# Performance work log

Hardware: AMD Instinct MI355X
Metric: run time of the kernel (lower is better)

The kernel has to match this reference:

```python
import jax, jax.numpy as jnp
import numpy as np

C, NC, B, T, H, W = 64, 4, 4, 8, 96, 96
BT = B * T
_DN = ('NCDHW', 'OIDHW', 'NCDHW')


def setup_inputs() -> dict:
    key = jax.random.key(0)
    ks = jax.random.split(key, 16)
    r = lambda i, shape, s=0.02: jax.random.normal(ks[i], shape, jnp.float32) * s
    f32 = jnp.float32
    return {
        'x': jax.random.normal(ks[0], (BT, C, H, W), f32),
        't': T,
        'temporal_kernels': r(1, (NC, C)),            # (num_components, C) per-channel kernel scale
        'kernel_weights': jnp.ones((NC,), f32),
        'length_scales': jnp.ones((NC,), f32),
        'temporal_basis': r(2, (C, T)),               # (C, 8) learned temporal basis
        'sc_w1': r(3, (C // 8, C), 0.05), 'sc_b1': jnp.zeros((C // 8,), f32),
        'sc_w2': r(4, (2 * C, C // 8), 0.05), 'sc_b2': jnp.zeros((2 * C,), f32),
        'diff_w': r(5, (C, 1, 3, 1, 1), 0.1),         # depthwise temporal conv
        'diff_gamma': jnp.ones((C,), f32), 'diff_beta': jnp.zeros((C,), f32),
        'diff_mean': r(6, (C,), 0.1),
        'diff_var': jnp.ones((C,), f32) + 0.1 * jax.random.uniform(ks[7], (C,), f32),
        'unc_w1': r(8, (C // 4, C), 0.05), 'unc_b1': jnp.zeros((C // 4,), f32),
        'unc_w2': r(9, (2, C // 4), 0.05), 'unc_b2': jnp.zeros((2,), f32),
        'pool_w': r(10, (C, C, 3, 1, 1), 0.02), 'pool_b': jnp.zeros((C,), f32),
        'proj_w': r(11, (C, C), 0.05),                # spectral-normalized 1x1x1 conv
        'bn_gamma': jnp.ones((C,), f32), 'bn_beta': jnp.zeros((C,), f32),
        'bn_mean': r(12, (C,), 0.1),
        'bn_var': jnp.ones((C,), f32) + 0.1 * jax.random.uniform(ks[13], (C,), f32),
        'temperature': jnp.float32(1.0),
    }


def _bc(v):
    return v[None, :, None, None, None]


def reference(x, t, temporal_kernels, kernel_weights, length_scales, temporal_basis,
              sc_w1, sc_b1, sc_w2, sc_b2,
              diff_w, diff_gamma, diff_beta, diff_mean, diff_var,
              unc_w1, unc_b1, unc_w2, unc_b2,
              pool_w, pool_b, proj_w,
              bn_gamma, bn_beta, bn_mean, bn_var, temperature):
    bt, c, h, w = x.shape
    b = bt // t
    x5 = x.reshape(b, t, c, h, w).transpose(0, 2, 1, 3, 4)   # (b,c,t,h,w)

    # --- Gaussian process temporal attention: per-channel (t,t) RBF mixture kernel ---
    ti = jnp.arange(t, dtype=x.dtype)
    dt2 = (ti[:, None] - ti[None, :]) ** 2                    # (t,t)
    ls = jnp.exp(length_scales)                               # (nc,)
    rbf = jnp.exp(-dt2[None] / (2.0 * ls[:, None, None] ** 2))  # (nc,t,t)
    wts = jax.nn.softmax(kernel_weights)
    K = jnp.einsum('i,ic,ist->cst', wts, temporal_kernels, rbf)  # (c,t,t)
    gp = jnp.einsum('cst,bctn->bcsn', K, x5.reshape(b, c, t, h * w)).reshape(b, c, t, h, w)

    # --- stochastic temporal sampling (eval: deterministic importance mask) ---
    mask = jax.nn.softmax(temporal_basis.mean(axis=0))        # (t,)
    stoch = x5 * mask[None, None, :, None, None]

    # --- spatial covariance gate (global pooled MLP -> sigmoid gate) ---
    g = x5.mean(axis=(2, 3, 4))                               # (b,c)
    h1 = jax.nn.gelu(g @ sc_w1.T + sc_b1, approximate=False)
    cov = h1 @ sc_w2.T + sc_b2                                # (b,2c); second half = cov_var
    cov_w = jax.nn.sigmoid(cov[:, c:])[:, :, None, None, None]
    fused0 = gp * cov_w + stoch * (1.0 - cov_w)

    # --- diffusion: depthwise temporal conv + BN(eval) + GELU ---
    d = jax.lax.conv_general_dilated(fused0, diff_w, (1, 1, 1), ((1, 1), (0, 0), (0, 0)),
                                     dimension_numbers=_DN, feature_group_count=c)
    d = _bc(diff_gamma) * (d - _bc(diff_mean)) / jnp.sqrt(_bc(diff_var) + 1e-5) + _bc(diff_beta)
    d = jax.nn.gelu(d, approximate=False)

    # --- uncertainty head + precision-weighted fusion ---
    u = jax.nn.gelu(jnp.einsum('bcthw,oc->bothw', d, unc_w1) + _bc(unc_b1), approximate=False)
    u = jnp.einsum('bcthw,oc->bothw', u, unc_w2) + _bc(unc_b2)  # (b,2,t,h,w)
    mu, var = u[:, :1], u[:, 1:]
    prec = 1.0 / (var + 1e-6)
    fused = (mu * prec + d) / (prec + 1.0)

    # --- temporal pool: temporal conv then global spatial mean ---
    p = jax.lax.conv_general_dilated(fused, pool_w, (1, 1, 1), ((1, 1), (0, 0), (0, 0)),
                                     dimension_numbers=_DN) + _bc(pool_b)
    out = fused + p.mean(axis=(3, 4), keepdims=True)

    # --- spectral-normalized 1x1x1 projection + BN(eval) ---
    sigma = jnp.linalg.svd(proj_w, compute_uv=False)[0]
    out = jnp.einsum('bcthw,oc->bothw', out, proj_w / sigma)
    out = _bc(bn_gamma) * (out - _bc(bn_mean)) / jnp.sqrt(_bc(bn_var) + 1e-5) + _bc(bn_beta)

    out = out.transpose(0, 2, 1, 3, 4).reshape(bt, c, h, w)
    return x + jnp.tanh(temperature) * out
```

## Files before the change

kernel.cpp:

```cpp
#include <hip/hip_runtime.h>
#include <math.h>

#define C64 64
#define NCK 4
#define BB  4
#define TT  8
#define HH  96
#define WW  96
#define HW  9216
#define CHW (C64*HW)
#define NTILE 32
#define NBLK_PER_B (HW/NTILE)

#define OFF_GSUM 0
#define OFF_S    256
#define OFF_COVW 2304
#define OFF_K    2560
#define OFF_MASK 6656
#define OFF_AC   6664
#define OFF_BC   6728
#define OFF_P2   6792
#define OFF_B2   10888
#define OFF_BIAS3 10952
#define OFF_P2BF 13000
#define OFF_P2T  15048
#define OFF_POOLT 19144
#define ZERO_N   2304

typedef __attribute__((ext_vector_type(8))) short short8;
typedef __attribute__((ext_vector_type(4))) float f32x4;

__device__ __forceinline__ float gelu_f(float v) {
    return 0.5f * v * (1.0f + erff(v * 0.70710678118654752f));
}
__device__ __forceinline__ unsigned short f2bf(float f) {
    union { float f; unsigned int u; } v; v.f = f;
    unsigned int r = (v.u + 0x7fffu + ((v.u >> 16) & 1u)) >> 16;
    return (unsigned short)r;
}
__device__ __forceinline__ float bf2f(unsigned short h) {
    union { unsigned int u; float f; } v; v.u = ((unsigned int)h) << 16;
    return v.f;
}
__device__ __forceinline__ int swz(int tn, int c) {
    return (tn << 6) + (c ^ ((tn & 7) << 3));
}

__global__ __launch_bounds__(256) void k1_gsum(const float* __restrict__ x,
                                               float* __restrict__ ws) {
    const int blk = blockIdx.x;
    const float4* p = reinterpret_cast<const float4*>(x + (size_t)blk * HW);
    float s = 0.f;
    for (int i = threadIdx.x; i < HW / 4; i += 256) {
        float4 v = p[i];
        s += v.x + v.y + v.z + v.w;
    }
    #pragma unroll
    for (int off = 32; off; off >>= 1) s += __shfl_down(s, off, 64);
    __shared__ float part[4];
    const int wid = threadIdx.x >> 6, lane = threadIdx.x & 63;
    if (lane == 0) part[wid] = s;
    __syncthreads();
    if (threadIdx.x == 0) {
        float t = part[0] + part[1] + part[2] + part[3];
        int c = blk % C64;
        int b = (blk / C64) / TT;
        atomicAdd(ws + OFF_GSUM + b * C64 + c, t);
    }
}

__global__ __launch_bounds__(256) void k2_prep(
    const float* __restrict__ tk, const float* __restrict__ kw,
    const float* __restrict__ lsc, const float* __restrict__ tb,
    const float* __restrict__ sc_w1, const float* __restrict__ sc_b1,
    const float* __restrict__ sc_w2, const float* __restrict__ sc_b2,
    const float* __restrict__ diff_gamma, const float* __restrict__ diff_beta,
    const float* __restrict__ diff_mean, const float* __restrict__ diff_var,
    const float* __restrict__ proj_w, const float* __restrict__ pool_w,
    const float* __restrict__ bn_gamma, const float* __restrict__ bn_beta,
    const float* __restrict__ bn_mean, const float* __restrict__ bn_var,
    const float* __restrict__ temperature,
    float* __restrict__ ws) {
    __shared__ float gsh[BB * C64];
    __shared__ float h1[BB][8];
    __shared__ float wtss[NCK], lss[NCK];
    __shared__ float Pls[64 * 64];
    __shared__ float Msh[64 * 64];
    __shared__ float M2sh[64 * 64];
    __shared__ float v0[64], v1[64];
    __shared__ float lamsh;
    const int tid = threadIdx.x;

    gsh[tid] = ws[OFF_GSUM + tid] * (1.0f / ((float)TT * (float)HW));
    for (int q = tid; q < 4096; q += 256) Pls[q] = proj_w[q];
    __syncthreads();

    if (tid < BB * 8) {
        int b = tid >> 3, j = tid & 7;
        float a = sc_b1[j];
        for (int c = 0; c < C64; c++) a += gsh[b * C64 + c] * sc_w1[j * C64 + c];
        h1[b][j] = gelu_f(a);
    }
    if (tid == 0) {
        float mx = -1e30f;
        for (int i = 0; i < NCK; i++) mx = fmaxf(mx, kw[i]);
        float e[NCK], s = 0.f;
        for (int i = 0; i < NCK; i++) { e[i] = expf(kw[i] - mx); s += e[i]; }
        for (int i = 0; i < NCK; i++) { wtss[i] = e[i] / s; lss[i] = expf(lsc[i]); }
    }
    if (tid == 1) {
        float m[TT], mx = -1e30f;
        for (int t = 0; t < TT; t++) {
            float a = 0.f;
            for (int c = 0; c < C64; c++) a += tb[c * TT + t];
            m[t] = a * (1.0f / (float)C64);
            mx = fmaxf(mx, m[t]);
        }
        float s = 0.f;
        for (int t = 0; t < TT; t++) { m[t] = expf(m[t] - mx); s += m[t]; }
        for (int t = 0; t < TT; t++) ws[OFF_MASK + t] = m[t] / s;
    }
    __syncthreads();

    {
        int b = tid >> 6, c = tid & 63;
        float a = sc_b2[C64 + c];
        for (int j = 0; j < 8; j++) a += h1[b][j] * sc_w2[(C64 + c) * 8 + j];
        ws[OFF_COVW + b * C64 + c] = 1.f / (1.f + expf(-a));
    }
    for (int q = tid; q < C64 * TT * TT; q += 256) {
        int c = q >> 6, s8 = (q >> 3) & 7, t8 = q & 7;
        float dt = (float)(s8 - t8);
        float dt2 = dt * dt;
        float a = 0.f;
        for (int i = 0; i < NCK; i++)
            a += wtss[i] * tk[i * C64 + c] * expf(-dt2 / (2.f * lss[i] * lss[i]));
        ws[OFF_K + (q & 63) * C64 + c] = a;
    }
    if (tid < C64) {
        float ac = diff_gamma[tid] * rsqrtf(diff_var[tid] + 1e-5f);
        ws[OFF_AC + tid] = ac;
        ws[OFF_BC + tid] = diff_beta[tid] - ac * diff_mean[tid];
    }
    for (int q = tid; q < C64 * C64 * 3; q += 256) {
        int o = q / 192, r = q % 192, cp = r / 3, k = r % 3;
        ws[OFF_POOLT + (k * C64 + cp) * C64 + o] = pool_w[q];
    }
    for (int q = tid; q < 4096; q += 256) {
        int i = q >> 6, j = q & 63;
        float a = 0.f;
        for (int k = 0; k < 64; k++) a += Pls[k * 64 + i] * Pls[k * 64 + j];
        Msh[q] = a;
    }
    __syncthreads();
    for (int q = tid; q < 4096; q += 256) {
        int i = q >> 6, j = q & 63;
        float a = 0.f;
        for (int k = 0; k < 64; k++) a += Msh[i * 64 + k] * Msh[k * 64 + j];
        M2sh[q] = a;
    }
    if (tid < 64) v0[tid] = 1.f;
    __syncthreads();
    for (int it = 0; it < 24; ++it) {
        float y = 0.f;
        if (tid < 64) {
            for (int k = 0; k < 64; k++) y += M2sh[k * 64 + tid] * v0[k];
        }
        float yy = y * y;
        #pragma unroll
        for (int off = 32; off; off >>= 1) yy += __shfl_down(yy, off, 64);
        float nrm = __shfl(yy, 0, 64);
        if (tid < 64) v1[tid] = y * rsqrtf(fmaxf(nrm, 1e-30f));
        __syncthreads();
        if (tid < 64) v0[tid] = v1[tid];
        __syncthreads();
    }
    {
        float a = 0.f;
        if (tid < 64) {
            for (int k = 0; k < 64; k++) a += Msh[k * 64 + tid] * v0[k];
            a *= v0[tid];
        }
        #pragma unroll
        for (int off = 32; off; off >>= 1) a += __shfl_down(a, off, 64);
        if (tid == 0) lamsh = a;
    }
    __syncthreads();
    const float sigma = sqrtf(fmaxf(lamsh, 1e-30f));
    const float tau = tanhf(temperature[0]);
    if (tid < 64) {
        float gp = bn_gamma[tid] * rsqrtf(bn_var[tid] + 1e-5f);
        ws[OFF_B2 + tid] = tau * (bn_beta[tid] - gp * bn_mean[tid]);
    }
    {
        short* p2b = (short*)(ws + OFF_P2BF);
        for (int q = tid; q < 4096; q += 256) {
            int o = q >> 6, c = q & 63;
            float gp = bn_gamma[o] * rsqrtf(bn_var[o] + 1e-5f);
            float v = tau * gp * Pls[q] / sigma;
            ws[OFF_P2 + q] = v;
            ws[OFF_P2T + c * C64 + o] = v;
            p2b[q] = (short)f2bf(v);
        }
    }
}

__global__ __launch_bounds__(256, 4) void k3_main(
    const float* __restrict__ x, const float* __restrict__ diff_w,
    const float* __restrict__ unc_w1, const float* __restrict__ unc_b1,
    const float* __restrict__ unc_w2, const float* __restrict__ unc_b2,
    const float* __restrict__ ws, float* __restrict__ out) {
    __shared__ short dls[256 * 64];
    const int tile = blockIdx.x;
    const int b = tile / NBLK_PER_B;
    const int n0 = (tile % NBLK_PER_B) * NTILE;
    const int tid = threadIdx.x;

    {
        const int cc = tid >> 2;
        const int nq = tid & 3;
        const float cw = ws[OFF_COVW + b * C64 + cc];
        const float ac = ws[OFF_AC + cc], bc = ws[OFF_BC + cc];
        const float w0 = diff_w[cc * 3 + 0], w1 = diff_w[cc * 3 + 1], w2 = diff_w[cc * 3 + 2];
        float mk[TT];
        #pragma unroll
        for (int t = 0; t < TT; t++) mk[t] = ws[OFF_MASK + t];
        #pragma unroll
        for (int q = 0; q < 2; ++q) {
            const int nb = q * 16 + nq * 4;
            float4 xr[TT];
            #pragma unroll
            for (int t = 0; t < TT; t++)
                xr[t] = *reinterpret_cast<const float4*>(
                    x + (size_t)((b * TT + t) * C64 + cc) * HW + n0 + nb);
            float f0[TT][4];
            #pragma unroll
            for (int s = 0; s < TT; s++) {
                float a0 = 0.f, a1 = 0.f, a2 = 0.f, a3 = 0.f;
                #pragma unroll
                for (int t = 0; t < TT; t++) {
                    const float kv = ws[OFF_K + (s * TT + t) * C64 + cc];
                    a0 += kv * xr[t].x; a1 += kv * xr[t].y;
                    a2 += kv * xr[t].z; a3 += kv * xr[t].w;
                }
                const float sm = mk[s] * (1.f - cw);
                f0[s][0] = a0 * cw + xr[s].x * sm;
                f0[s][1] = a1 * cw + xr[s].y * sm;
                f0[s][2] = a2 * cw + xr[s].z * sm;
                f0[s][3] = a3 * cw + xr[s].w * sm;
            }
            #pragma unroll
            for (int t = 0; t < TT; t++) {
                #pragma unroll
                for (int i = 0; i < 4; i++) {
                    float pre = w1 * f0[t][i];
                    if (t > 0)      pre += w0 * f0[t - 1][i];
                    if (t < TT - 1) pre += w2 * f0[t + 1][i];
                    dls[swz(t * 32 + nb + i, cc)] = (short)f2bf(gelu_f(ac * pre + bc));
                }
            }
        }
    }
    __syncthreads();

    {
        const int t = tid >> 5;
        float u1[16];
        #pragma unroll
        for (int o = 0; o < 16; o++) u1[o] = unc_b1[o];
        #pragma unroll
        for (int j = 0; j < 8; j++) {
            short8 v = *(const short8*)(dls + swz(tid, j * 8));
            #pragma unroll
            for (int i = 0; i < 8; i++) {
                const float dv = bf2f((unsigned short)v[i]);
                #pragma unroll
                for (int o = 0; o < 16; o++)
                    u1[o] += unc_w1[o * C64 + j * 8 + i] * dv;
            }
        }
        #pragma unroll
        for (int o = 0; o < 16; o++) u1[o] = gelu_f(u1[o]);
        float mu = unc_b2[0], va = unc_b2[1];
        #pragma unroll
        for (int o = 0; o < 16; o++) {
            mu += unc_w2[o] * u1[o];
            va += unc_w2[16 + o] * u1[o];
        }
        const float vp = va + 1e-6f;
        const float inv = 1.f / (1.f + vp);
        const float alpha = vp * inv;
        const float beta = mu * inv;

        #pragma unroll
        for (int j = 0; j < 8; j++) {
            short8 v = *(const short8*)(dls + swz(tid, j * 8));
            short8 wv;
            #pragma unroll
            for (int i = 0; i < 8; i++) {
                const float f = alpha * bf2f((unsigned short)v[i]) + beta;
                wv[i] = (short)f2bf(f);
                float s = f;
                s += __shfl_xor(s, 1);
                s += __shfl_xor(s, 2);
                s += __shfl_xor(s, 4);
                s += __shfl_xor(s, 8);
                s += __shfl_xor(s, 16);
                if ((tid & 31) == 0)
                    atomicAdd((float*)ws + OFF_S + (b * C64 + (j * 8 + i)) * TT + t, s);
            }
            *(short8*)(dls + swz(tid, j * 8)) = wv;
        }
    }
    __syncthreads();

    {
        const int w = tid >> 6;
        const int l = tid & 63;
        const int l15 = l & 15;
        const int lg = (l >> 4) & 3;
        const short* P2B = (const short*)(ws + OFF_P2BF);
        f32x4 acc[4][4] = {};
        #pragma unroll
        for (int kh = 0; kh < 2; ++kh) {
            const int cb = kh * 32 + lg * 8;
            short8 bfr[4];
            #pragma unroll
            for (int nt = 0; nt < 4; ++nt) {
                const int tn = w * 64 + nt * 16 + l15;
                bfr[nt] = *(const short8*)(dls + swz(tn, cb));
            }
            #pragma unroll
            for (int mt = 0; mt < 4; ++mt) {
                const int o = mt * 16 + l15;
                short8 afr = *(const short8*)(P2B + o * 64 + cb);
                #pragma unroll
                for (int nt = 0; nt < 4; ++nt)
                    acc[mt][nt] = __builtin_amdgcn_mfma_f32_16x16x32_bf16(
                        afr, bfr[nt], acc[mt][nt], 0, 0, 0);
            }
        }
        #pragma unroll
        for (int nt = 0; nt < 4; ++nt) {
            const int t = 2 * w + (nt >> 1);
            const int nl = (nt & 1) * 16 + l15;
            #pragma unroll
            for (int mt = 0; mt < 4; ++mt) {
                #pragma unroll
                for (int j = 0; j < 4; ++j) {
                    const int o = mt * 16 + lg * 4 + j;
                    const size_t idx = (size_t)((b * TT + t) * C64 + o) * HW + n0 + nl;
                    out[idx] = x[idx] + acc[mt][nt][j];
                }
            }
        }
    }
}

__global__ __launch_bounds__(64) void k4_bias(
    const float* __restrict__ pool_b, float* __restrict__ ws) {
    const int b = blockIdx.x >> 3, t = blockIdx.x & 7;
    const int o = threadIdx.x;
    __shared__ float pm[C64];
    float a = 0.f;
    for (int k = 0; k < 3; k++) {
        int tt = t + k - 1;
        if (tt < 0 || tt >= TT) continue;
        const float* Pk = ws + OFF_POOLT + k * C64 * C64;
        const float* Sp = ws + OFF_S + b * C64 * TT + tt;
        for (int cp = 0; cp < C64; cp++)
            a += Pk[cp * C64 + o] * Sp[cp * TT];
    }
    pm[o] = pool_b[o] + a * (1.0f / (float)HW);
    __syncthreads();
    float bb = ws[OFF_B2 + o];
    for (int c = 0; c < C64; c++) bb += ws[OFF_P2T + c * C64 + o] * pm[c];
    ws[OFF_BIAS3 + (b * C64 + o) * TT + t] = bb;
}

__global__ __launch_bounds__(256) void k5_bias(
    const float* __restrict__ ws, float* __restrict__ out) {
    const int plane = blockIdx.x;
    const int o = plane & 63;
    const int bt = plane >> 6;
    const int b = bt >> 3, t = bt & 7;
    const float bias = ws[OFF_BIAS3 + (b * C64 + o) * TT + t];
    float4* p = reinterpret_cast<float4*>(out + (size_t)plane * HW);
    #pragma unroll
    for (int i = 0; i < 9; i++) {
        const int idx = threadIdx.x + i * 256;
        float4 v = p[idx];
        v.x += bias; v.y += bias; v.z += bias; v.w += bias;
        p[idx] = v;
    }
}

extern "C" void kernel_launch(void* const* d_in, const int* in_sizes, int n_in,
                              void* d_out, int out_size, void* d_ws, size_t ws_size,
                              hipStream_t stream) {
    const float* x           = (const float*)d_in[0];
    const float* tk          = (const float*)d_in[2];
    const float* kw          = (const float*)d_in[3];
    const float* lsc         = (const float*)d_in[4];
    const float* tb          = (const float*)d_in[5];
    const float* sc_w1       = (const float*)d_in[6];
    const float* sc_b1       = (const float*)d_in[7];
    const float* sc_w2       = (const float*)d_in[8];
    const float* sc_b2       = (const float*)d_in[9];
    const float* diff_w      = (const float*)d_in[10];
    const float* diff_gamma  = (const float*)d_in[11];
    const float* diff_beta   = (const float*)d_in[12];
    const float* diff_mean   = (const float*)d_in[13];
    const float* diff_var    = (const float*)d_in[14];
    const float* unc_w1      = (const float*)d_in[15];
    const float* unc_b1      = (const float*)d_in[16];
    const float* unc_w2      = (const float*)d_in[17];
    const float* unc_b2      = (const float*)d_in[18];
    const float* pool_w      = (const float*)d_in[19];
    const float* pool_b      = (const float*)d_in[20];
    const float* proj_w      = (const float*)d_in[21];
    const float* bn_gamma    = (const float*)d_in[22];
    const float* bn_beta     = (const float*)d_in[23];
    const float* bn_mean     = (const float*)d_in[24];
    const float* bn_var      = (const float*)d_in[25];
    const float* temperature = (const float*)d_in[26];
    float* ws = (float*)d_ws;
    float* out = (float*)d_out;

    hipMemsetAsync(ws, 0, ZERO_N * sizeof(float), stream);
    k1_gsum<<<dim3(BB * TT * C64), dim3(256), 0, stream>>>(x, ws);
    k2_prep<<<dim3(1), dim3(256), 0, stream>>>(tk, kw, lsc, tb, sc_w1, sc_b1,
                                               sc_w2, sc_b2, diff_gamma, diff_beta,
                                               diff_mean, diff_var, proj_w, pool_w,
                                               bn_gamma, bn_beta, bn_mean, bn_var,
                                               temperature, ws);
    k3_main<<<dim3(BB * NBLK_PER_B), dim3(256), 0, stream>>>(x, diff_w, unc_w1, unc_b1,
                                                             unc_w2, unc_b2, ws, out);
    k4_bias<<<dim3(BB * TT), dim3(64), 0, stream>>>(pool_b, ws);
    k5_bias<<<dim3(BB * TT * C64), dim3(256), 0, stream>>>(ws, out);
}
```

Measured before the change: 562.5 us.

## Reshape main kernel thread mapping to cut registers and parallelize bias reduction

New measurement: 535.8 us. 1.05x faster.

```diff
diff --git a/kernel.cpp b/kernel.cpp
--- a/kernel.cpp
+++ b/kernel.cpp
@@ -205,7 +205,7 @@
     }
 }
 
-__global__ __launch_bounds__(256, 4) void k3_main(
+__global__ __launch_bounds__(256) void k3_main(
     const float* __restrict__ x, const float* __restrict__ diff_w,
     const float* __restrict__ unc_w1, const float* __restrict__ unc_b1,
     const float* __restrict__ unc_w2, const float* __restrict__ unc_b2,
@@ -215,49 +215,37 @@
     const int b = tile / NBLK_PER_B;
     const int n0 = (tile % NBLK_PER_B) * NTILE;
     const int tid = threadIdx.x;
-
-    {
-        const int cc = tid >> 2;
-        const int nq = tid & 3;
-        const float cw = ws[OFF_COVW + b * C64 + cc];
-        const float ac = ws[OFF_AC + cc], bc = ws[OFF_BC + cc];
-        const float w0 = diff_w[cc * 3 + 0], w1 = diff_w[cc * 3 + 1], w2 = diff_w[cc * 3 + 2];
+    const int nloc = tid & 31;
+
+    {
+        const int n = n0 + nloc;
         float mk[TT];
         #pragma unroll
         for (int t = 0; t < TT; t++) mk[t] = ws[OFF_MASK + t];
         #pragma unroll
-        for (int q = 0; q < 2; ++q) {
-            const int nb = q * 16 + nq * 4;
-            float4 xr[TT];
+        for (int p = 0; p < 8; p++) {
+            const int c = (tid >> 5) + (p << 3);
+            float xr[TT];
             #pragma unroll
             for (int t = 0; t < TT; t++)
-                xr[t] = *reinterpret_cast<const float4*>(
-                    x + (size_t)((b * TT + t) * C64 + cc) * HW + n0 + nb);
-            float f0[TT][4];
+                xr[t] = x[(size_t)((b * TT + t) * C64 + c) * HW + n];
+            const float cw = ws[OFF_COVW + b * C64 + c];
+            float f0[TT];
             #pragma unroll
             for (int s = 0; s < TT; s++) {
-                float a0 = 0.f, a1 = 0.f, a2 = 0.f, a3 = 0.f;
+                float a = 0.f;
                 #pragma unroll
-                for (int t = 0; t < TT; t++) {
-                    const float kv = ws[OFF_K + (s * TT + t) * C64 + cc];
-                    a0 += kv * xr[t].x; a1 += kv * xr[t].y;
-                    a2 += kv * xr[t].z; a3 += kv * xr[t].w;
-                }
-                const float sm = mk[s] * (1.f - cw);
-                f0[s][0] = a0 * cw + xr[s].x * sm;
-                f0[s][1] = a1 * cw + xr[s].y * sm;
-                f0[s][2] = a2 * cw + xr[s].z * sm;
-                f0[s][3] = a3 * cw + xr[s].w * sm;
-            }
+                for (int t = 0; t < TT; t++) a += ws[OFF_K + (s * TT + t) * C64 + c] * xr[t];
+                f0[s] = a * cw + xr[s] * mk[s] * (1.f - cw);
+            }
+            const float w0 = diff_w[c * 3 + 0], w1 = diff_w[c * 3 + 1], w2 = diff_w[c * 3 + 2];
+            const float ac = ws[OFF_AC + c], bc = ws[OFF_BC + c];
             #pragma unroll
             for (int t = 0; t < TT; t++) {
-                #pragma unroll
-                for (int i = 0; i < 4; i++) {
-                    float pre = w1 * f0[t][i];
-                    if (t > 0)      pre += w0 * f0[t - 1][i];
-                    if (t < TT - 1) pre += w2 * f0[t + 1][i];
-                    dls[swz(t * 32 + nb + i, cc)] = (short)f2bf(gelu_f(ac * pre + bc));
-                }
+                float pre = w1 * f0[t];
+                if (t > 0)      pre += w0 * f0[t - 1];
+                if (t < TT - 1) pre += w2 * f0[t + 1];
+                dls[swz(t * 32 + nloc, c)] = (short)f2bf(gelu_f(ac * pre + bc));
             }
         }
     }
@@ -320,47 +308,42 @@
         const int l15 = l & 15;
         const int lg = (l >> 4) & 3;
         const short* P2B = (const short*)(ws + OFF_P2BF);
-        f32x4 acc[4][4] = {};
-        #pragma unroll
-        for (int kh = 0; kh < 2; ++kh) {
-            const int cb = kh * 32 + lg * 8;
-            short8 bfr[4];
-            #pragma unroll
-            for (int nt = 0; nt < 4; ++nt) {
-                const int tn = w * 64 + nt * 16 + l15;
-                bfr[nt] = *(const short8*)(dls + swz(tn, cb));
-            }
-            #pragma unroll
-            for (int mt = 0; mt < 4; ++mt) {
+        #pragma unroll
+        for (int mt = 0; mt < 4; ++mt) {
+            f32x4 acc[4] = {};
+            #pragma unroll
+            for (int kh = 0; kh < 2; ++kh) {
+                const int cb = kh * 32 + lg * 8;
                 const int o = mt * 16 + l15;
                 short8 afr = *(const short8*)(P2B + o * 64 + cb);
                 #pragma unroll
-                for (int nt = 0; nt < 4; ++nt)
-                    acc[mt][nt] = __builtin_amdgcn_mfma_f32_16x16x32_bf16(
-                        afr, bfr[nt], acc[mt][nt], 0, 0, 0);
-            }
-        }
-        #pragma unroll
-        for (int nt = 0; nt < 4; ++nt) {
-            const int t = 2 * w + (nt >> 1);
-            const int nl = (nt & 1) * 16 + l15;
-            #pragma unroll
-            for (int mt = 0; mt < 4; ++mt) {
+                for (int nt = 0; nt < 4; ++nt) {
+                    const int tn = w * 64 + nt * 16 + l15;
+                    short8 bfr = *(const short8*)(dls + swz(tn, cb));
+                    acc[nt] = __builtin_amdgcn_mfma_f32_16x16x32_bf16(
+                        afr, bfr, acc[nt], 0, 0, 0);
+                }
+            }
+            #pragma unroll
+            for (int nt = 0; nt < 4; ++nt) {
+                const int t = 2 * w + (nt >> 1);
+                const int nl = (nt & 1) * 16 + l15;
                 #pragma unroll
                 for (int j = 0; j < 4; ++j) {
                     const int o = mt * 16 + lg * 4 + j;
                     const size_t idx = (size_t)((b * TT + t) * C64 + o) * HW + n0 + nl;
-                    out[idx] = x[idx] + acc[mt][nt][j];
+                    out[idx] = x[idx] + acc[nt][j];
                 }
             }
         }
     }
 }
 
-__global__ __launch_bounds__(64) void k4_bias(
+__global__ __launch_bounds__(256) void k4_bias(
     const float* __restrict__ pool_b, float* __restrict__ ws) {
     const int b = blockIdx.x >> 3, t = blockIdx.x & 7;
-    const int o = threadIdx.x;
+    const int o = threadIdx.x >> 2, q = threadIdx.x & 3;
+    __shared__ float part[256];
     __shared__ float pm[C64];
     float a = 0.f;
     for (int k = 0; k < 3; k++) {
@@ -368,14 +351,22 @@
         if (tt < 0 || tt >= TT) continue;
         const float* Pk = ws + OFF_POOLT + k * C64 * C64;
         const float* Sp = ws + OFF_S + b * C64 * TT + tt;
-        for (int cp = 0; cp < C64; cp++)
+        for (int cp = q * 16; cp < q * 16 + 16; cp++)
             a += Pk[cp * C64 + o] * Sp[cp * TT];
     }
-    pm[o] = pool_b[o] + a * (1.0f / (float)HW);
-    __syncthreads();
-    float bb = ws[OFF_B2 + o];
-    for (int c = 0; c < C64; c++) bb += ws[OFF_P2T + c * C64 + o] * pm[c];
-    ws[OFF_BIAS3 + (b * C64 + o) * TT + t] = bb;
+    part[threadIdx.x] = a;
+    __syncthreads();
+    if (q == 0)
+        pm[o] = pool_b[o] + (part[o * 4] + part[o * 4 + 1] + part[o * 4 + 2] + part[o * 4 + 3])
+                            * (1.0f / (float)HW);
+    __syncthreads();
+    float bb = 0.f;
+    for (int c = q * 16; c < q * 16 + 16; c++) bb += ws[OFF_P2T + c * C64 + o] * pm[c];
+    part[threadIdx.x] = bb;
+    __syncthreads();
+    if (q == 0)
+        ws[OFF_BIAS3 + (b * C64 + o) * TT + t] =
+            ws[OFF_B2 + o] + part[o * 4] + part[o * 4 + 1] + part[o * 4 + 2] + part[o * 4 + 3];
 }
 
 __global__ __launch_bounds__(256) void k5_bias(
@@ -436,6 +427,6 @@
                                                temperature, ws);
     k3_main<<<dim3(BB * NBLK_PER_B), dim3(256), 0, stream>>>(x, diff_w, unc_w1, unc_b1,
                                                              unc_w2, unc_b2, ws, out);
-    k4_bias<<<dim3(BB * TT), dim3(64), 0, stream>>>(pool_b, ws);
+    k4_bias<<<dim3(BB * TT), dim3(256), 0, stream>>>(pool_b, ws);
     k5_bias<<<dim3(BB * TT * C64), dim3(256), 0, stream>>>(ws, out);
 }
```
